# Kernel optimization log

Hardware: AMD Instinct MI355X
Metric: run time of the kernel (lower is better)

The kernel has to match this reference:

```python
import jax, jax.numpy as jnp
import numpy as np


def setup_inputs() -> dict:
    key = jax.random.key(0)
    ks = jax.random.split(key, 5)
    B, C, H, W = 4, 64, 64, 64
    C8 = C // 8
    return {
        "x_opt": jax.random.normal(ks[0], (B, C, H, W), jnp.float32),
        "x_sar": jax.random.normal(ks[1], (B, C, H, W), jnp.float32),
        "wq": jax.random.normal(ks[2], (C8, C), jnp.float32) * 0.05,
        "bq": jnp.zeros((C8,), jnp.float32),
        "wk": jax.random.normal(ks[3], (C8, C), jnp.float32) * 0.05,
        "bk": jnp.zeros((C8,), jnp.float32),
        "wv": jax.random.normal(ks[4], (C, C), jnp.float32) * 0.05,
        "bv": jnp.zeros((C,), jnp.float32),
        "gamma": jnp.zeros((1,), jnp.float32),
    }


def reference(x_opt, x_sar, wq, bq, wk, bk, wv, bv, gamma):
    b, c, h, w = x_opt.shape
    n = h * w
    xo = x_opt.reshape(b, c, n)  # [b, c, N]
    xs = x_sar.reshape(b, c, n)
    # 1x1 convs == channel matmuls
    q = jnp.einsum('oc,bcn->bon', wq, xo) + bq[None, :, None]  # [b, c//8, N]
    k = jnp.einsum('oc,bcn->bon', wk, xs) + bk[None, :, None]  # [b, c//8, N]
    v = jnp.einsum('oc,bcn->bon', wv, xs) + bv[None, :, None]  # [b, c, N]
    # attn[b, n, m] = softmax_m( q[:, :, n] . k[:, :, m] )  -- NO 1/sqrt(d) scaling
    scores = jnp.einsum('bdn,bdm->bnm', q, k)  # [b, N, N]
    attn = jax.nn.softmax(scores, axis=-1)
    # out[b, c, n] = sum_m v[b, c, m] * attn[b, n, m]
    out = jnp.einsum('bcm,bnm->bcn', v, attn).reshape(b, c, h, w)
    return gamma[0] * out + x_opt
```

## Files before the change

kernel.cpp:

```cpp
#include <hip/hip_runtime.h>
#include <hip/hip_bf16.h>
#include <stdint.h>

#define NDIM 4096
#define CDIM 64
#define NSPLIT 8
#define SPAN (NDIM / NSPLIT)
#define NQ4 (SPAN / 32)
#define LOG2E 1.44269504088896f

typedef float f32x4 __attribute__((ext_vector_type(4)));
typedef float f32x16 __attribute__((ext_vector_type(16)));
typedef short bf16x8 __attribute__((ext_vector_type(8)));
union U4B { uint4 u; bf16x8 b; };

static __device__ __forceinline__ uint32_t cvtpk(float lo, float hi) {
  uint32_t r;
  asm("v_cvt_pk_bf16_f32 %0, %1, %2" : "=v"(r) : "v"(lo), "v"(hi));
  return r;
}
static __device__ __forceinline__ uint16_t f2bf(float f) {
  uint32_t r;
  asm("v_cvt_pk_bf16_f32 %0, %1, %1" : "=v"(r) : "v"(f));
  return (uint16_t)r;
}
static __device__ __forceinline__ float fexp2(float x) {
  return __builtin_amdgcn_exp2f(x);
}

__global__ __launch_bounds__(256) void proj_kernel(
    const float* __restrict__ x_opt, const float* __restrict__ x_sar,
    const float* __restrict__ wq, const float* __restrict__ bq,
    const float* __restrict__ wk, const float* __restrict__ bk,
    const float* __restrict__ wvp, const float* __restrict__ bv,
    uint16_t* __restrict__ qf, uint16_t* __restrict__ kfp,
    uint16_t* __restrict__ vf2)
{
  const int tid = threadIdx.x;
  const int w = tid >> 6;
  const int l = tid & 63;
  const int x = l & 31;
  const int hi = l >> 5;

  const int id = blockIdx.x;
  const int b = id >> 7;
  const int n0 = (id & 127) * 32;
  const size_t xbase = (size_t)b * CDIM * NDIM;

  const float* xsrc = (w == 2) ? x_opt : x_sar;
  bf16x8 xB[4];
#pragma unroll
  for (int kc = 0; kc < 4; kc++) {
    float sv[8];
#pragma unroll
    for (int j = 0; j < 8; j++)
      sv[j] = xsrc[xbase + (size_t)(kc * 16 + hi * 8 + j) * NDIM + n0 + x];
    U4B us;
    us.u = make_uint4(cvtpk(sv[0], sv[1]), cvtpk(sv[2], sv[3]),
                      cvtpk(sv[4], sv[5]), cvtpk(sv[6], sv[7]));
    xB[kc] = us.b;
  }

  bf16x8 aF[4];
#pragma unroll
  for (int kc = 0; kc < 4; kc++) {
    U4B ua;
    ua.u = make_uint4(0u, 0u, 0u, 0u);
    if (w < 2) {
      const float* wr = wvp + (w * 32 + x) * 64 + kc * 16 + hi * 8;
      float4 wa = ((const float4*)wr)[0];
      float4 wb = ((const float4*)wr)[1];
      ua.u = make_uint4(cvtpk(wa.x, wa.y), cvtpk(wa.z, wa.w),
                        cvtpk(wb.x, wb.y), cvtpk(wb.z, wb.w));
    } else if (x < 8) {
      const float* wr = ((w == 2) ? wq : wk) + x * 64 + kc * 16 + hi * 8;
      float4 wa = ((const float4*)wr)[0];
      float4 wb = ((const float4*)wr)[1];
      ua.u = make_uint4(cvtpk(wa.x, wa.y), cvtpk(wa.z, wa.w),
                        cvtpk(wb.x, wb.y), cvtpk(wb.z, wb.w));
    }
    aF[kc] = ua.b;
  }

  const f32x16 z16 = {0.f,0.f,0.f,0.f, 0.f,0.f,0.f,0.f,
                      0.f,0.f,0.f,0.f, 0.f,0.f,0.f,0.f};
  f32x16 acc = z16;
#pragma unroll
  for (int kc = 0; kc < 4; kc++)
    acc = __builtin_amdgcn_mfma_f32_32x32x16_bf16(aF[kc], xB[kc], acc, 0, 0, 0);

  if (w < 2) {
    const size_t kbbase = (size_t)b * 256 + (n0 >> 4) + (x >> 4);
    const int kk = x & 15;
#pragma unroll
    for (int r = 0; r < 16; r++) {
      const int row = w * 32 + (r & 3) + 8 * (r >> 2) + 4 * hi;
      vf2[(kbbase * 64 + row) * 16 + kk] = f2bf(acc[r] + bv[row]);
    }
  } else if (w == 2) {
    float gv[4];
#pragma unroll
    for (int r = 0; r < 4; r++) gv[r] = (acc[r] + bq[4 * hi + r]) * LOG2E;
    const size_t nrow = ((size_t)b * NDIM + n0 + x) * 16;
    uint2 st;
    st.x = cvtpk(gv[0], gv[1]); st.y = cvtpk(gv[2], gv[3]);
    *(uint2*)(qf + nrow + hi * 4) = st;
    if (hi == 0) {
      const uint4 z4 = make_uint4(0u, 0u, 0u, 0u);
      *(uint4*)(qf + nrow + 8) = z4;
    }
  } else {
    float gv[4];
#pragma unroll
    for (int r = 0; r < 4; r++) gv[r] = acc[r] + bk[4 * hi + r];
    uint2 st;
    st.x = cvtpk(gv[0], gv[1]); st.y = cvtpk(gv[2], gv[3]);
    *(uint2*)(kfp + ((size_t)b * NDIM + n0 + x) * 8 + hi * 4) = st;
  }
}

__global__ __launch_bounds__(256, 4) void attn_kernel(
    const uint16_t* __restrict__ qf, const uint16_t* __restrict__ kfp,
    const uint16_t* __restrict__ vf2,
    uint16_t* __restrict__ po2, float* __restrict__ ls)
{
  const int tid = threadIdx.x;
  const int w = tid >> 6;
  const int l = tid & 63;
  const int x = l & 31;
  const int hi = l >> 5;

  const int id = blockIdx.x;
  const int sp = id & 7;
  const int qb = (id >> 3) & 31;
  const int b = id >> 8;

  const int n0 = qb * 128;
  const int qrow = n0 + w * 32 + x;

  U4B qfr;
  qfr.u = *(const uint4*)(qf + ((size_t)b * NDIM + qrow) * 16 + hi * 8);

  const uint16_t* kbase = kfp + ((size_t)b * NDIM + sp * SPAN + x) * 8;
  const uint16_t* vbase =
      vf2 + (((size_t)b * 256 + sp * 32) * 64 + x) * 16 + hi * 8;

  const f32x16 z16 = {0.f,0.f,0.f,0.f, 0.f,0.f,0.f,0.f,
                      0.f,0.f,0.f,0.f, 0.f,0.f,0.f,0.f};
  f32x16 oacc0 = z16, oacc1 = z16;
  float lacc[4] = {0.f, 0.f, 0.f, 0.f};

  uint4 kc   = *(const uint4*)(kbase);
  uint4 va00 = *(const uint4*)(vbase);
  uint4 va01 = *(const uint4*)(vbase + 512);
  uint4 va10 = *(const uint4*)(vbase + 1024);
  uint4 va11 = *(const uint4*)(vbase + 1536);

#pragma unroll
  for (int gq = 0; gq < NQ4; gq++) {
    const int vo = (gq + 1) * 2048;
    uint4 kn   = *(const uint4*)(kbase + (gq + 1) * 256);
    uint4 vn00 = *(const uint4*)(vbase + vo);
    uint4 vn01 = *(const uint4*)(vbase + vo + 512);
    uint4 vn10 = *(const uint4*)(vbase + vo + 1024);
    uint4 vn11 = *(const uint4*)(vbase + vo + 1536);

    U4B ka; ka.u = kc;
    f32x16 s = __builtin_amdgcn_mfma_f32_32x32x16_bf16(ka.b, qfr.b, z16, 0, 0, 0);

    uint32_t W[8];
#pragma unroll
    for (int j = 0; j < 8; j++) {
      const float p0 = fexp2(s[2 * j]);
      const float p1 = fexp2(s[2 * j + 1]);
      W[j] = cvtpk(p0, p1);
      lacc[j & 3] += p0 + p1;
    }

    __builtin_amdgcn_s_setprio(1);
    {
      uint32_t a0 = W[0], b0 = W[2], a1 = W[1], b1 = W[3];
      asm("v_permlane32_swap_b32 %0, %1" : "+v"(a0), "+v"(b0));
      asm("v_permlane32_swap_b32 %0, %1" : "+v"(a1), "+v"(b1));
      U4B pf, va, vb;
      pf.u = make_uint4(a0, a1, b0, b1);
      va.u = va00; vb.u = va01;
      oacc0 = __builtin_amdgcn_mfma_f32_32x32x16_bf16(va.b, pf.b, oacc0, 0, 0, 0);
      oacc1 = __builtin_amdgcn_mfma_f32_32x32x16_bf16(vb.b, pf.b, oacc1, 0, 0, 0);
    }
    {
      uint32_t a0 = W[4], b0 = W[6], a1 = W[5], b1 = W[7];
      asm("v_permlane32_swap_b32 %0, %1" : "+v"(a0), "+v"(b0));
      asm("v_permlane32_swap_b32 %0, %1" : "+v"(a1), "+v"(b1));
      U4B pf, va, vb;
      pf.u = make_uint4(a0, a1, b0, b1);
      va.u = va10; vb.u = va11;
      oacc0 = __builtin_amdgcn_mfma_f32_32x32x16_bf16(va.b, pf.b, oacc0, 0, 0, 0);
      oacc1 = __builtin_amdgcn_mfma_f32_32x32x16_bf16(vb.b, pf.b, oacc1, 0, 0, 0);
    }
    __builtin_amdgcn_s_setprio(0);

    kc = kn; va00 = vn00; va01 = vn01; va10 = vn10; va11 = vn11;
  }

  {
    uint16_t* pb = po2 + ((size_t)(sp * 256 + b * 64 + hi * 4)) * NDIM + qrow;
#pragma unroll
    for (int r = 0; r < 16; r++) {
      const size_t off = (size_t)((r & 3) + 8 * (r >> 2)) * NDIM;
      pb[off] = f2bf(oacc0[r]);
      pb[off + (size_t)32 * NDIM] = f2bf(oacc1[r]);
    }
  }
  float ltot = (lacc[0] + lacc[1]) + (lacc[2] + lacc[3]);
  ltot += __shfl_xor(ltot, 32);
  if (hi == 0)
    ls[((size_t)sp * 4 + b) * NDIM + qrow] = ltot;
}

__global__ __launch_bounds__(256) void merge_kernel(
    const uint16_t* __restrict__ po2, const float* __restrict__ ls,
    const float* __restrict__ x_opt, const float* __restrict__ gamma,
    float* __restrict__ out)
{
  const int idx = blockIdx.x * 256 + threadIdx.x;
  const int n8 = (idx & 511) << 3;
  const int row = idx >> 9;
  const int b = row >> 6;

  float acc[8] = {0.f, 0.f, 0.f, 0.f, 0.f, 0.f, 0.f, 0.f};
  f32x4 ws0 = {0.f, 0.f, 0.f, 0.f};
  f32x4 ws1 = {0.f, 0.f, 0.f, 0.f};
#pragma unroll
  for (int s = 0; s < NSPLIT; s++) {
    const uint4 pv = *(const uint4*)(po2 + ((size_t)s * 256 + row) * NDIM + n8);
    const uint32_t* pw = (const uint32_t*)&pv;
#pragma unroll
    for (int j = 0; j < 4; j++) {
      acc[j * 2 + 0] += __uint_as_float(pw[j] << 16);
      acc[j * 2 + 1] += __uint_as_float(pw[j] & 0xFFFF0000u);
    }
    const float* lp = ls + ((size_t)s * 4 + b) * NDIM + n8;
    ws0 += *(const f32x4*)(lp);
    ws1 += *(const f32x4*)(lp + 4);
  }
  const float gm = gamma[0];
  const float* xp = x_opt + (size_t)row * NDIM + n8;
  float* op = out + (size_t)row * NDIM + n8;
  float4 x0 = ((const float4*)xp)[0];
  float4 x1 = ((const float4*)xp)[1];
  float4 o0, o1;
  o0.x = gm * acc[0] / ws0[0] + x0.x;
  o0.y = gm * acc[1] / ws0[1] + x0.y;
  o0.z = gm * acc[2] / ws0[2] + x0.z;
  o0.w = gm * acc[3] / ws0[3] + x0.w;
  o1.x = gm * acc[4] / ws1[0] + x1.x;
  o1.y = gm * acc[5] / ws1[1] + x1.y;
  o1.z = gm * acc[6] / ws1[2] + x1.z;
  o1.w = gm * acc[7] / ws1[3] + x1.w;
  ((float4*)op)[0] = o0;
  ((float4*)op)[1] = o1;
}

extern "C" void kernel_launch(void* const* d_in, const int* in_sizes, int n_in,
                              void* d_out, int out_size, void* d_ws, size_t ws_size,
                              hipStream_t stream) {
  const float* x_opt = (const float*)d_in[0];
  const float* x_sar = (const float*)d_in[1];
  const float* wq    = (const float*)d_in[2];
  const float* bq    = (const float*)d_in[3];
  const float* wk    = (const float*)d_in[4];
  const float* bk    = (const float*)d_in[5];
  const float* wvp   = (const float*)d_in[6];
  const float* bv    = (const float*)d_in[7];
  const float* gamma = (const float*)d_in[8];
  float* outp = (float*)d_out;

  uint16_t* qf  = (uint16_t*)d_ws;
  uint16_t* kfp = (uint16_t*)((char*)d_ws + 524288);
  uint16_t* vf2 = (uint16_t*)((char*)d_ws + 1048576);
  uint16_t* po2 = (uint16_t*)((char*)d_ws + 3145728);
  float* lsp    = (float*)((char*)d_ws + 19922944);

  proj_kernel<<<512, 256, 0, stream>>>(x_opt, x_sar, wq, bq, wk, bk, wvp, bv,
                                       qf, kfp, vf2);
  attn_kernel<<<1024, 256, 0, stream>>>(qf, kfp, vf2, po2, lsp);
  merge_kernel<<<512, 256, 0, stream>>>(po2, lsp, x_opt, gamma, outp);
}
```

Measured before the change: 36.66 us.

## Stage K/V tiles into LDS via async global_load_lds with double buffering

The attention kernel now loads K and V tiles once per block into shared memory with direct global-to-LDS loads, double-buffered across 64-key tiles. Before, each of the four waves fetched the same K/V data into registers on its own. The V layout written by the projection kernel changes to match the LDS tile layout. This cuts redundant global and L2 traffic but adds a block-wide barrier per tile and LDS reads, which could slow progress if waves stall.

```diff
diff --git a/kernel.cpp b/kernel.cpp
--- a/kernel.cpp
+++ b/kernel.cpp
@@ -6,7 +6,7 @@
 #define CDIM 64
 #define NSPLIT 8
 #define SPAN (NDIM / NSPLIT)
-#define NQ4 (SPAN / 32)
+#define NT (SPAN / 64)
 #define LOG2E 1.44269504088896f
 
 typedef float f32x4 __attribute__((ext_vector_type(4)));
@@ -26,6 +26,11 @@
 }
 static __device__ __forceinline__ float fexp2(float x) {
   return __builtin_amdgcn_exp2f(x);
+}
+static __device__ __forceinline__ void gload_lds16(const void* g, void* l) {
+  __builtin_amdgcn_global_load_lds(
+      (const __attribute__((address_space(1))) uint32_t*)g,
+      (__attribute__((address_space(3))) uint32_t*)l, 16, 0, 0);
 }
 
 __global__ __launch_bounds__(256) void proj_kernel(
@@ -34,7 +39,7 @@
     const float* __restrict__ wk, const float* __restrict__ bk,
     const float* __restrict__ wvp, const float* __restrict__ bv,
     uint16_t* __restrict__ qf, uint16_t* __restrict__ kfp,
-    uint16_t* __restrict__ vf2)
+    uint16_t* __restrict__ vf3)
 {
   const int tid = threadIdx.x;
   const int w = tid >> 6;
@@ -90,12 +95,13 @@
     acc = __builtin_amdgcn_mfma_f32_32x32x16_bf16(aF[kc], xB[kc], acc, 0, 0, 0);
 
   if (w < 2) {
-    const size_t kbbase = (size_t)b * 256 + (n0 >> 4) + (x >> 4);
-    const int kk = x & 15;
+    const size_t qbase =
+        (((size_t)b * 128 + (n0 >> 5)) * 4 + (x >> 3)) * 64;
+    const int kslot = x & 7;
 #pragma unroll
     for (int r = 0; r < 16; r++) {
       const int row = w * 32 + (r & 3) + 8 * (r >> 2) + 4 * hi;
-      vf2[(kbbase * 64 + row) * 16 + kk] = f2bf(acc[r] + bv[row]);
+      vf3[(qbase + row) * 8 + kslot] = f2bf(acc[r] + bv[row]);
     }
   } else if (w == 2) {
     float gv[4];
@@ -121,9 +127,11 @@
 
 __global__ __launch_bounds__(256, 4) void attn_kernel(
     const uint16_t* __restrict__ qf, const uint16_t* __restrict__ kfp,
-    const uint16_t* __restrict__ vf2,
+    const uint16_t* __restrict__ vf3,
     uint16_t* __restrict__ po2, float* __restrict__ ls)
 {
+  __shared__ __align__(16) uint8_t smem[18432];
+
   const int tid = threadIdx.x;
   const int w = tid >> 6;
   const int l = tid & 63;
@@ -141,66 +149,69 @@
   U4B qfr;
   qfr.u = *(const uint4*)(qf + ((size_t)b * NDIM + qrow) * 16 + hi * 8);
 
-  const uint16_t* kbase = kfp + ((size_t)b * NDIM + sp * SPAN + x) * 8;
-  const uint16_t* vbase =
-      vf2 + (((size_t)b * 256 + sp * 32) * 64 + x) * 16 + hi * 8;
+  const uint16_t* vsrc = vf3 + ((size_t)b * 128 + sp * 16) * 2048;
+  const uint16_t* ksrc = kfp + ((size_t)b * NDIM + sp * SPAN) * 8;
+
+  const int vlane = hi * 1024 + x * 16;
+  const int klane = x * 16;
+
+  auto stageTile = [&](int t, int nbuf) {
+    const uint16_t* sv = vsrc + (size_t)t * 4096;
+    uint8_t* dv = smem + nbuf * 8192;
+    gload_lds16(sv + (2 * w) * 512 + l * 8, dv + (2 * w) * 1024);
+    gload_lds16(sv + (2 * w + 1) * 512 + l * 8, dv + (2 * w + 1) * 1024);
+    if (w == 3)
+      gload_lds16(ksrc + (size_t)t * 512 + l * 8, smem + 16384 + nbuf * 1024);
+  };
 
   const f32x16 z16 = {0.f,0.f,0.f,0.f, 0.f,0.f,0.f,0.f,
                       0.f,0.f,0.f,0.f, 0.f,0.f,0.f,0.f};
   f32x16 oacc0 = z16, oacc1 = z16;
   float lacc[4] = {0.f, 0.f, 0.f, 0.f};
 
-  uint4 kc   = *(const uint4*)(kbase);
-  uint4 va00 = *(const uint4*)(vbase);
-  uint4 va01 = *(const uint4*)(vbase + 512);
-  uint4 va10 = *(const uint4*)(vbase + 1024);
-  uint4 va11 = *(const uint4*)(vbase + 1536);
-
-#pragma unroll
-  for (int gq = 0; gq < NQ4; gq++) {
-    const int vo = (gq + 1) * 2048;
-    uint4 kn   = *(const uint4*)(kbase + (gq + 1) * 256);
-    uint4 vn00 = *(const uint4*)(vbase + vo);
-    uint4 vn01 = *(const uint4*)(vbase + vo + 512);
-    uint4 vn10 = *(const uint4*)(vbase + vo + 1024);
-    uint4 vn11 = *(const uint4*)(vbase + vo + 1536);
-
-    U4B ka; ka.u = kc;
-    f32x16 s = __builtin_amdgcn_mfma_f32_32x32x16_bf16(ka.b, qfr.b, z16, 0, 0, 0);
-
-    uint32_t W[8];
-#pragma unroll
-    for (int j = 0; j < 8; j++) {
-      const float p0 = fexp2(s[2 * j]);
-      const float p1 = fexp2(s[2 * j + 1]);
-      W[j] = cvtpk(p0, p1);
-      lacc[j & 3] += p0 + p1;
-    }
-
-    __builtin_amdgcn_s_setprio(1);
-    {
-      uint32_t a0 = W[0], b0 = W[2], a1 = W[1], b1 = W[3];
-      asm("v_permlane32_swap_b32 %0, %1" : "+v"(a0), "+v"(b0));
-      asm("v_permlane32_swap_b32 %0, %1" : "+v"(a1), "+v"(b1));
-      U4B pf, va, vb;
-      pf.u = make_uint4(a0, a1, b0, b1);
-      va.u = va00; vb.u = va01;
-      oacc0 = __builtin_amdgcn_mfma_f32_32x32x16_bf16(va.b, pf.b, oacc0, 0, 0, 0);
-      oacc1 = __builtin_amdgcn_mfma_f32_32x32x16_bf16(vb.b, pf.b, oacc1, 0, 0, 0);
-    }
-    {
-      uint32_t a0 = W[4], b0 = W[6], a1 = W[5], b1 = W[7];
-      asm("v_permlane32_swap_b32 %0, %1" : "+v"(a0), "+v"(b0));
-      asm("v_permlane32_swap_b32 %0, %1" : "+v"(a1), "+v"(b1));
-      U4B pf, va, vb;
-      pf.u = make_uint4(a0, a1, b0, b1);
-      va.u = va10; vb.u = va11;
-      oacc0 = __builtin_amdgcn_mfma_f32_32x32x16_bf16(va.b, pf.b, oacc0, 0, 0, 0);
-      oacc1 = __builtin_amdgcn_mfma_f32_32x32x16_bf16(vb.b, pf.b, oacc1, 0, 0, 0);
-    }
-    __builtin_amdgcn_s_setprio(0);
-
-    kc = kn; va00 = vn00; va01 = vn01; va10 = vn10; va11 = vn11;
+  stageTile(0, 0);
+  __syncthreads();
+
+#pragma unroll
+  for (int t = 0; t < NT; t++) {
+    const int buf = t & 1;
+    if (t + 1 < NT) stageTile(t + 1, buf ^ 1);
+    const uint8_t* vb = smem + buf * 8192;
+    const uint8_t* kb = smem + 16384 + buf * 1024;
+
+#pragma unroll
+    for (int h = 0; h < 2; h++) {
+      U4B ka;
+      ka.u = *(const uint4*)(kb + h * 512 + klane);
+      f32x16 s = __builtin_amdgcn_mfma_f32_32x32x16_bf16(ka.b, qfr.b, z16, 0, 0, 0);
+
+      uint32_t W[8];
+#pragma unroll
+      for (int j = 0; j < 8; j++) {
+        const float p0 = fexp2(s[2 * j]);
+        const float p1 = fexp2(s[2 * j + 1]);
+        W[j] = cvtpk(p0, p1);
+        lacc[j & 3] += p0 + p1;
+      }
+
+      __builtin_amdgcn_s_setprio(1);
+#pragma unroll
+      for (int sub = 0; sub < 2; sub++) {
+        uint32_t a0 = W[sub * 4 + 0], b0 = W[sub * 4 + 2];
+        uint32_t a1 = W[sub * 4 + 1], b1 = W[sub * 4 + 3];
+        asm("v_permlane32_swap_b32 %0, %1" : "+v"(a0), "+v"(b0));
+        asm("v_permlane32_swap_b32 %0, %1" : "+v"(a1), "+v"(b1));
+        U4B pf, va, vc;
+        pf.u = make_uint4(a0, a1, b0, b1);
+        const int ko4 = (h * 4 + sub * 2) * 1024;
+        va.u = *(const uint4*)(vb + ko4 + vlane);
+        vc.u = *(const uint4*)(vb + ko4 + 512 + vlane);
+        oacc0 = __builtin_amdgcn_mfma_f32_32x32x16_bf16(va.b, pf.b, oacc0, 0, 0, 0);
+        oacc1 = __builtin_amdgcn_mfma_f32_32x32x16_bf16(vc.b, pf.b, oacc1, 0, 0, 0);
+      }
+      __builtin_amdgcn_s_setprio(0);
+    }
+    __syncthreads();
   }
 
   {
@@ -278,12 +289,12 @@
 
   uint16_t* qf  = (uint16_t*)d_ws;
   uint16_t* kfp = (uint16_t*)((char*)d_ws + 524288);
-  uint16_t* vf2 = (uint16_t*)((char*)d_ws + 1048576);
+  uint16_t* vf3 = (uint16_t*)((char*)d_ws + 1048576);
   uint16_t* po2 = (uint16_t*)((char*)d_ws + 3145728);
   float* lsp    = (float*)((char*)d_ws + 19922944);
 
   proj_kernel<<<512, 256, 0, stream>>>(x_opt, x_sar, wq, bq, wk, bk, wvp, bv,
-                                       qf, kfp, vf2);
-  attn_kernel<<<1024, 256, 0, stream>>>(qf, kfp, vf2, po2, lsp);
+                                       qf, kfp, vf3);
+  attn_kernel<<<1024, 256, 0, stream>>>(qf, kfp, vf3, po2, lsp);
   merge_kernel<<<512, 256, 0, stream>>>(po2, lsp, x_opt, gamma, outp);
 }
```

Result: slower. 66.46 us (+81.3%).
